# Performance work log

Measured on AMD Instinct MI355X. Metric: run time of the kernel, lower is better.

## Reference

```python
import math
import jax, jax.numpy as jnp
import numpy as np

NUM_CODE = 4096
CODE_DIM = 256
IN_DIM = 1024

def chi_dist_mean_std(c):
    mean = math.sqrt(2.0) * math.exp(math.lgamma((c + 1) / 2) - math.lgamma(c / 2))
    std = math.sqrt(c - mean ** 2)
    return mean, std

MU, SIGMA = chi_dist_mean_std(CODE_DIM)


def setup_inputs() -> dict:
    key = jax.random.key(0)
    k1, k2, k3 = jax.random.split(key, 3)
    encode = jax.random.normal(k1, (8, 64, 64, CODE_DIM), dtype=jnp.float32)
    codebook_w = jax.random.normal(k2, (NUM_CODE, IN_DIM), dtype=jnp.float32)  # N(0,1) init
    proj_w = jax.random.normal(k3, (CODE_DIM, IN_DIM), dtype=jnp.float32) * (1.0 / math.sqrt(IN_DIM))
    proj_b = jnp.zeros((CODE_DIM,), dtype=jnp.float32)
    return {"encode": encode, "codebook_w": codebook_w, "proj_w": proj_w, "proj_b": proj_b}


def _cdist(z, e):
    # pairwise euclidean distance: [T, K]
    z2 = jnp.sum(z * z, axis=-1, keepdims=True)          # [T,1]
    e2 = jnp.sum(e * e, axis=-1)[None, :]                # [1,K]
    d2 = z2 + e2 - 2.0 * jnp.einsum('tc,kc->tk', z, e)
    return jnp.sqrt(jnp.maximum(d2, 0.0))


def reference(encode, codebook_w, proj_w, proj_b):
    b, h, w, c = encode.shape
    e = codebook_w @ proj_w.T + proj_b                   # [K, code_dim]
    z = encode.reshape(-1, c)                            # [T, code_dim]
    s = -_cdist(z, e)                                    # [T, K] (computed under no_grad in torch)
    simi = (s.reshape(b, h, w, -1) - MU) / SIGMA
    zsoft = jax.nn.softmax(simi, axis=-1)                # eval path (std=0)
    zidx = jnp.argmax(zsoft, axis=-1)                    # [b,h,w]
    quant = e[zidx]                                      # [b,h,w,code_dim]
    return (zidx, quant)
```

## Files before the change

kernel.cpp:

```cpp
#include <hip/hip_runtime.h>
#include <hip/hip_bf16.h>


#define K_CODES 4096
#define CDIM    256
#define IDIM    1024
#define NTOK    32768

typedef __attribute__((ext_vector_type(8))) short short8;
typedef __attribute__((ext_vector_type(4))) float f32x4;

__device__ __forceinline__ unsigned short f32_to_bf16_rne(float f) {
  union { float f; unsigned int u; } x; x.f = f;
  unsigned int r = x.u + 0x7FFFu + ((x.u >> 16) & 1u);
  return (unsigned short)(r >> 16);
}
__device__ __forceinline__ float bf16_to_f32(unsigned short h) {
  union { unsigned int u; float f; } x; x.u = ((unsigned int)h) << 16;
  return x.f;
}

extern "C" __global__ __launch_bounds__(512)
void proj_gemm(const float* __restrict__ cb, const float* __restrict__ pw,
               const float* __restrict__ pb, float* __restrict__ e,
               unsigned short* __restrict__ Ect, float* __restrict__ e2p) {
  __shared__ float As[32][68];
  __shared__ float Bs[32][68];
  const int tid = threadIdx.x;
  const int tx = tid & 15, ty = tid >> 4;
  const int m0 = blockIdx.y << 6;
  const int n0 = blockIdx.x << 6;
  const int r  = tid >> 3;
  const int c4 = (tid & 7) << 2;
  float acc[2][4] = {};
  for (int k0 = 0; k0 < IDIM; k0 += 32) {
    float4 a0 = *(const float4*)&cb[(size_t)(m0 + r) * IDIM + k0 + c4];
    float4 b0 = *(const float4*)&pw[(size_t)(n0 + r) * IDIM + k0 + c4];
    __syncthreads();
    As[c4+0][r]=a0.x; As[c4+1][r]=a0.y; As[c4+2][r]=a0.z; As[c4+3][r]=a0.w;
    Bs[c4+0][r]=b0.x; Bs[c4+1][r]=b0.y; Bs[c4+2][r]=b0.z; Bs[c4+3][r]=b0.w;
    __syncthreads();
    #pragma unroll
    for (int kk = 0; kk < 32; ++kk) {
      const float2 av = *(const float2*)&As[kk][ty*2];
      const float4 bv = *(const float4*)&Bs[kk][tx*4];
      const float a2[2] = {av.x, av.y};
      const float b4[4] = {bv.x, bv.y, bv.z, bv.w};
      #pragma unroll
      for (int i = 0; i < 2; ++i)
        #pragma unroll
        for (int j = 0; j < 4; ++j)
          acc[i][j] += a2[i] * b4[j];
    }
  }
  const int col0 = n0 + tx*4;
  const int kb   = col0 >> 5;
  const int g    = (col0 >> 3) & 3;
  const int half = (col0 >> 2) & 1;
  float p2[2];
  #pragma unroll
  for (int i = 0; i < 2; ++i) {
    const int row = m0 + ty*2 + i;
    float vv[4];
    unsigned short h4[4], l4[4];
    #pragma unroll
    for (int j = 0; j < 4; ++j) {
      vv[j] = acc[i][j] + pb[col0 + j];
      h4[j] = f32_to_bf16_rne(vv[j]);
      l4[j] = f32_to_bf16_rne(vv[j] - bf16_to_f32(h4[j]));
    }
    *(float4*)&e[(size_t)row * CDIM + col0] = *(float4*)vv;
    const int ct = row >> 4, cl = row & 15;
    const size_t fi = ((size_t)(kb      * 256 + ct) * 64 + g*16 + cl) * 8 + half*4;
    const size_t fo = ((size_t)((kb+8)  * 256 + ct) * 64 + g*16 + cl) * 8 + half*4;
    *(ushort4*)&Ect[fi] = *(ushort4*)h4;
    *(ushort4*)&Ect[fo] = *(ushort4*)l4;
    p2[i] = vv[0]*vv[0] + vv[1]*vv[1] + vv[2]*vv[2] + vv[3]*vv[3];
  }
  #pragma unroll
  for (int m = 1; m < 16; m <<= 1) {
    p2[0] += __shfl_xor(p2[0], m, 64);
    p2[1] += __shfl_xor(p2[1], m, 64);
  }
  if (tx == 0) {
    e2p[(size_t)blockIdx.x * K_CODES + m0 + ty*2    ] = p2[0];
    e2p[(size_t)blockIdx.x * K_CODES + m0 + ty*2 + 1] = p2[1];
  }
}

extern "C" __global__ __launch_bounds__(512, 2)
void score_mfma(const float* __restrict__ z, const unsigned short* __restrict__ Ect,
                const float* __restrict__ e2p, const float* __restrict__ eg,
                float* __restrict__ zidx_f, float* __restrict__ quant) {
  extern __shared__ __align__(16) char smem[];
  char* Zb = smem;

  const int tid = threadIdx.x;
  const int l   = tid & 63;
  const int w   = tid >> 6;
  const int tg  = w >> 2;
  const int cg  = w & 3;
  const int t0  = blockIdx.x << 7;

  #pragma unroll
  for (int rr = 0; rr < 2; ++rr) {
    const int r  = rr*64 + (tid >> 3);
    const int cq = tid & 7;
    const int i8 = r >> 4;
    const int rl = (r & 15) << 4;
    #pragma unroll
    for (int it = 0; it < 4; ++it) {
      const int col = cq*32 + it*8;
      const float4 v0 = *(const float4*)&z[(size_t)(t0 + r) * CDIM + col];
      const float4 v1 = *(const float4*)&z[(size_t)(t0 + r) * CDIM + col + 4];
      float vv[8] = {v0.x,v0.y,v0.z,v0.w,v1.x,v1.y,v1.z,v1.w};
      unsigned int hp[4], lp[4];
      #pragma unroll
      for (int c = 0; c < 4; ++c) {
        unsigned short h0 = f32_to_bf16_rne(vv[2*c]);
        unsigned short h1 = f32_to_bf16_rne(vv[2*c+1]);
        unsigned short l0 = f32_to_bf16_rne(vv[2*c]   - bf16_to_f32(h0));
        unsigned short l1 = f32_to_bf16_rne(vv[2*c+1] - bf16_to_f32(h1));
        hp[c] = (unsigned int)h0 | ((unsigned int)h1 << 16);
        lp[c] = (unsigned int)l0 | ((unsigned int)l1 << 16);
      }
      const int lane_b = it*256 + rl;
      *(uint4*)(Zb + (size_t)(i8*16 + cq    ) * 1024 + lane_b) = *(uint4*)hp;
      *(uint4*)(Zb + (size_t)(i8*16 + cq + 8) * 1024 + lane_b) = *(uint4*)lp;
    }
  }
  __syncthreads();

  float bestv[4][4];
  int   besti[4][4];
  #pragma unroll
  for (int i = 0; i < 4; ++i)
    #pragma unroll
    for (int r = 0; r < 4; ++r) { bestv[i][r] = 3.4e38f; besti[i][r] = 0; }

  const int cl = l & 15;
  const int g  = l >> 4;

  const char* ebase = (const char*)Ect + (size_t)l * 16 + (size_t)cg * 4096;
  const char* Zl    = Zb + (size_t)l * 16 + (size_t)tg * 65536;

  short8 aHc[4], aLc[4], bHc[4], bLc[4];
  #pragma unroll
  for (int i = 0; i < 4; ++i) {
    aHc[i] = *(const short8*)(Zl + (size_t)(i*16 + 0) * 1024);
    aLc[i] = *(const short8*)(Zl + (size_t)(i*16 + 8) * 1024);
  }
  #pragma unroll
  for (int jj = 0; jj < 4; ++jj) {
    bHc[jj] = *(const short8*)(ebase + (size_t)0 * 262144 + jj * 1024);
    bLc[jj] = *(const short8*)(ebase + (size_t)8 * 262144 + jj * 1024);
  }

  for (int cc = 0; cc < 16; ++cc) {
    const char* ecc  = ebase + (size_t)cc * 16384;
    const char* eccn = ebase + (size_t)((cc + 1) & 15) * 16384;

    f32x4 acc[4][4];
    #pragma unroll
    for (int i = 0; i < 4; ++i)
      #pragma unroll
      for (int jj = 0; jj < 4; ++jj) acc[i][jj] = (f32x4){0.f,0.f,0.f,0.f};

    float e2v[4];
    #pragma unroll
    for (int jj = 0; jj < 4; ++jj) {
      const int code = cc*256 + cg*64 + jj*16 + cl;
      e2v[jj] = e2p[code] + e2p[K_CODES + code]
              + e2p[2*K_CODES + code] + e2p[3*K_CODES + code];
    }

    #pragma unroll
    for (int kw = 0; kw < 8; ++kw) {
      short8 aHn[4], aLn[4], bHn[4], bLn[4];
      {
        const char* bsrc = (kw < 7) ? ecc : eccn;
        const int kwn = (kw + 1) & 7;
        #pragma unroll
        for (int jj = 0; jj < 4; ++jj) {
          bHn[jj] = *(const short8*)(bsrc + (size_t)(kwn    ) * 262144 + jj * 1024);
          bLn[jj] = *(const short8*)(bsrc + (size_t)(kwn + 8) * 262144 + jj * 1024);
        }
        #pragma unroll
        for (int i = 0; i < 4; ++i) {
          aHn[i] = *(const short8*)(Zl + (size_t)(i*16 + kwn    ) * 1024);
          aLn[i] = *(const short8*)(Zl + (size_t)(i*16 + kwn + 8) * 1024);
        }
      }
      __builtin_amdgcn_s_setprio(1);
      #pragma unroll
      for (int i = 0; i < 4; ++i)
        #pragma unroll
        for (int jj = 0; jj < 4; ++jj)
          acc[i][jj] = __builtin_amdgcn_mfma_f32_16x16x32_bf16(aHc[i], bHc[jj], acc[i][jj], 0, 0, 0);
      #pragma unroll
      for (int i = 0; i < 4; ++i)
        #pragma unroll
        for (int jj = 0; jj < 4; ++jj)
          acc[i][jj] = __builtin_amdgcn_mfma_f32_16x16x32_bf16(aHc[i], bLc[jj], acc[i][jj], 0, 0, 0);
      #pragma unroll
      for (int i = 0; i < 4; ++i)
        #pragma unroll
        for (int jj = 0; jj < 4; ++jj)
          acc[i][jj] = __builtin_amdgcn_mfma_f32_16x16x32_bf16(aLc[i], bHc[jj], acc[i][jj], 0, 0, 0);
      __builtin_amdgcn_s_setprio(0);
      #pragma unroll
      for (int i = 0; i < 4; ++i) { aHc[i] = aHn[i]; aLc[i] = aLn[i]; }
      #pragma unroll
      for (int jj = 0; jj < 4; ++jj) { bHc[jj] = bHn[jj]; bLc[jj] = bLn[jj]; }
    }
    #pragma unroll
    for (int jj = 0; jj < 4; ++jj) {
      const int code = cc*256 + cg*64 + jj*16 + cl;
      #pragma unroll
      for (int i = 0; i < 4; ++i)
        #pragma unroll
        for (int r = 0; r < 4; ++r) {
          const float sc = e2v[jj] - 2.0f * acc[i][jj][r];
          if (sc < bestv[i][r]) { bestv[i][r] = sc; besti[i][r] = code; }
        }
    }
  }

  struct RP { float v; int i; };
  RP*  red    = (RP*)(smem + 131072);
  int* sh_idx = (int*)(smem + 131072 + 4096);
  #pragma unroll
  for (int i = 0; i < 4; ++i)
    #pragma unroll
    for (int r = 0; r < 4; ++r) {
      float v = bestv[i][r]; int bi = besti[i][r];
      #pragma unroll
      for (int m = 1; m < 16; m <<= 1) {
        const float ov = __shfl_xor(v, m, 64);
        const int   oi = __shfl_xor(bi, m, 64);
        if (ov < v || (ov == v && oi < bi)) { v = ov; bi = oi; }
      }
      if (cl == 0) {
        const int tl = tg*64 + i*16 + g*4 + r;
        red[tl*4 + cg].v = v; red[tl*4 + cg].i = bi;
      }
    }
  __syncthreads();
  if (tid < 128) {
    float v = red[tid*4].v; int bi = red[tid*4].i;
    #pragma unroll
    for (int x = 1; x < 4; ++x) {
      const float ov = red[tid*4 + x].v; const int oi = red[tid*4 + x].i;
      if (ov < v || (ov == v && oi < bi)) { v = ov; bi = oi; }
    }
    zidx_f[t0 + tid] = (float)bi;
    sh_idx[tid] = bi;
  }
  __syncthreads();

  #pragma unroll
  for (int rr = 0; rr < 2; ++rr) {
    const int r   = rr*64 + (tid >> 3);
    const int cq  = (tid & 7) << 5;
    const int idx = sh_idx[r];
    #pragma unroll
    for (int it = 0; it < 4; ++it) {
      const float4 v0 = *(const float4*)&eg[(size_t)idx * CDIM + cq + it*8];
      const float4 v1 = *(const float4*)&eg[(size_t)idx * CDIM + cq + it*8 + 4];
      *(float4*)&quant[(size_t)(t0 + r) * CDIM + cq + it*8]     = v0;
      *(float4*)&quant[(size_t)(t0 + r) * CDIM + cq + it*8 + 4] = v1;
    }
  }
}

extern "C" void kernel_launch(void* const* d_in, const int* in_sizes, int n_in,
                              void* d_out, int out_size, void* d_ws, size_t ws_size,
                              hipStream_t stream) {
  const float* encode = (const float*)d_in[0];
  const float* cb     = (const float*)d_in[1];
  const float* pw     = (const float*)d_in[2];
  const float* pb     = (const float*)d_in[3];

  float* e   = (float*)d_ws;
  float* e2p = e + (size_t)K_CODES * CDIM;
  unsigned short* Ect = (unsigned short*)(e2p + 4*K_CODES);

  float* out     = (float*)d_out;
  float* zidx_f  = out;
  float* quant_f = out + NTOK;

  (void)hipFuncSetAttribute((const void*)score_mfma,
                            hipFuncAttributeMaxDynamicSharedMemorySize, 135680);

  proj_gemm<<<dim3(CDIM/64, K_CODES/64), 512, 0, stream>>>(cb, pw, pb, e, Ect, e2p);
  score_mfma<<<NTOK/128, 512, 135680, stream>>>(encode, Ect, e2p, e, zidx_f, quant_f);
}
```

Measured before the change: 222.5 us.

## Split-K proj_gemm across two thread groups with 4x4 register tiles

The projection GEMM now splits the 1024-long reduction between two 256-thread halves of the block. Each thread computes a 4x4 output tile instead of 2x4, which raises arithmetic per shared-memory load. The two partial sums are combined through shared memory before the same epilogue (bias, bf16 hi/lo split, squared-norm partials). This aims to cut the loop trip count and improve register reuse, at the cost of more registers, a second shared buffer, and an extra reduction step with barriers.

Result: faster. 212.1 us (-4.7%).

```diff
diff --git a/kernel.cpp b/kernel.cpp
--- a/kernel.cpp
+++ b/kernel.cpp
@@ -24,67 +24,87 @@
 void proj_gemm(const float* __restrict__ cb, const float* __restrict__ pw,
                const float* __restrict__ pb, float* __restrict__ e,
                unsigned short* __restrict__ Ect, float* __restrict__ e2p) {
-  __shared__ float As[32][68];
-  __shared__ float Bs[32][68];
+  __shared__ float As[2][32][68];
+  __shared__ float Bs[2][32][68];
   const int tid = threadIdx.x;
-  const int tx = tid & 15, ty = tid >> 4;
-  const int m0 = blockIdx.y << 6;
-  const int n0 = blockIdx.x << 6;
-  const int r  = tid >> 3;
-  const int c4 = (tid & 7) << 2;
-  float acc[2][4] = {};
-  for (int k0 = 0; k0 < IDIM; k0 += 32) {
-    float4 a0 = *(const float4*)&cb[(size_t)(m0 + r) * IDIM + k0 + c4];
-    float4 b0 = *(const float4*)&pw[(size_t)(n0 + r) * IDIM + k0 + c4];
+  const int kg  = tid >> 8;
+  const int t   = tid & 255;
+  const int tx  = t & 15, ty = t >> 4;
+  const int m0  = blockIdx.y << 6;
+  const int n0  = blockIdx.x << 6;
+  const int r   = t >> 2;
+  const int c8  = (t & 3) << 3;
+  float acc[4][4] = {};
+  for (int k0s = 0; k0s < 16; ++k0s) {
+    const int k0 = kg*512 + k0s*32;
+    float4 a0 = *(const float4*)&cb[(size_t)(m0 + r) * IDIM + k0 + c8];
+    float4 a1 = *(const float4*)&cb[(size_t)(m0 + r) * IDIM + k0 + c8 + 4];
+    float4 b0 = *(const float4*)&pw[(size_t)(n0 + r) * IDIM + k0 + c8];
+    float4 b1 = *(const float4*)&pw[(size_t)(n0 + r) * IDIM + k0 + c8 + 4];
     __syncthreads();
-    As[c4+0][r]=a0.x; As[c4+1][r]=a0.y; As[c4+2][r]=a0.z; As[c4+3][r]=a0.w;
-    Bs[c4+0][r]=b0.x; Bs[c4+1][r]=b0.y; Bs[c4+2][r]=b0.z; Bs[c4+3][r]=b0.w;
+    As[kg][c8+0][r]=a0.x; As[kg][c8+1][r]=a0.y; As[kg][c8+2][r]=a0.z; As[kg][c8+3][r]=a0.w;
+    As[kg][c8+4][r]=a1.x; As[kg][c8+5][r]=a1.y; As[kg][c8+6][r]=a1.z; As[kg][c8+7][r]=a1.w;
+    Bs[kg][c8+0][r]=b0.x; Bs[kg][c8+1][r]=b0.y; Bs[kg][c8+2][r]=b0.z; Bs[kg][c8+3][r]=b0.w;
+    Bs[kg][c8+4][r]=b1.x; Bs[kg][c8+5][r]=b1.y; Bs[kg][c8+6][r]=b1.z; Bs[kg][c8+7][r]=b1.w;
     __syncthreads();
     #pragma unroll
     for (int kk = 0; kk < 32; ++kk) {
-      const float2 av = *(const float2*)&As[kk][ty*2];
-      const float4 bv = *(const float4*)&Bs[kk][tx*4];
-      const float a2[2] = {av.x, av.y};
+      const float4 av = *(const float4*)&As[kg][kk][ty*4];
+      const float4 bv = *(const float4*)&Bs[kg][kk][tx*4];
+      const float a4[4] = {av.x, av.y, av.z, av.w};
       const float b4[4] = {bv.x, bv.y, bv.z, bv.w};
       #pragma unroll
-      for (int i = 0; i < 2; ++i)
+      for (int i = 0; i < 4; ++i)
         #pragma unroll
         for (int j = 0; j < 4; ++j)
-          acc[i][j] += a2[i] * b4[j];
-    }
-  }
-  const int col0 = n0 + tx*4;
-  const int kb   = col0 >> 5;
-  const int g    = (col0 >> 3) & 3;
-  const int half = (col0 >> 2) & 1;
-  float p2[2];
-  #pragma unroll
-  for (int i = 0; i < 2; ++i) {
-    const int row = m0 + ty*2 + i;
-    float vv[4];
-    unsigned short h4[4], l4[4];
-    #pragma unroll
-    for (int j = 0; j < 4; ++j) {
-      vv[j] = acc[i][j] + pb[col0 + j];
-      h4[j] = f32_to_bf16_rne(vv[j]);
-      l4[j] = f32_to_bf16_rne(vv[j] - bf16_to_f32(h4[j]));
-    }
-    *(float4*)&e[(size_t)row * CDIM + col0] = *(float4*)vv;
-    const int ct = row >> 4, cl = row & 15;
-    const size_t fi = ((size_t)(kb      * 256 + ct) * 64 + g*16 + cl) * 8 + half*4;
-    const size_t fo = ((size_t)((kb+8)  * 256 + ct) * 64 + g*16 + cl) * 8 + half*4;
-    *(ushort4*)&Ect[fi] = *(ushort4*)h4;
-    *(ushort4*)&Ect[fo] = *(ushort4*)l4;
-    p2[i] = vv[0]*vv[0] + vv[1]*vv[1] + vv[2]*vv[2] + vv[3]*vv[3];
-  }
-  #pragma unroll
-  for (int m = 1; m < 16; m <<= 1) {
-    p2[0] += __shfl_xor(p2[0], m, 64);
-    p2[1] += __shfl_xor(p2[1], m, 64);
-  }
-  if (tx == 0) {
-    e2p[(size_t)blockIdx.x * K_CODES + m0 + ty*2    ] = p2[0];
-    e2p[(size_t)blockIdx.x * K_CODES + m0 + ty*2 + 1] = p2[1];
+          acc[i][j] += a4[i] * b4[j];
+    }
+  }
+  float* Cb = (float*)As;
+  __syncthreads();
+  if (kg == 1) {
+    #pragma unroll
+    for (int i = 0; i < 4; ++i)
+      *(float4*)&Cb[(ty*4 + i) * 64 + tx*4] = *(float4*)&acc[i][0];
+  }
+  __syncthreads();
+  if (kg == 0) {
+    const int col0 = n0 + tx*4;
+    const int kb   = col0 >> 5;
+    const int g    = (col0 >> 3) & 3;
+    const int half = (col0 >> 2) & 1;
+    float p2[4];
+    #pragma unroll
+    for (int i = 0; i < 4; ++i) {
+      const float4 o = *(const float4*)&Cb[(ty*4 + i) * 64 + tx*4];
+      const int row = m0 + ty*4 + i;
+      float vv[4];
+      unsigned short h4[4], l4[4];
+      const float o4[4] = {o.x, o.y, o.z, o.w};
+      #pragma unroll
+      for (int j = 0; j < 4; ++j) {
+        vv[j] = acc[i][j] + o4[j] + pb[col0 + j];
+        h4[j] = f32_to_bf16_rne(vv[j]);
+        l4[j] = f32_to_bf16_rne(vv[j] - bf16_to_f32(h4[j]));
+      }
+      *(float4*)&e[(size_t)row * CDIM + col0] = *(float4*)vv;
+      const int ct = row >> 4, cl = row & 15;
+      const size_t fi = ((size_t)(kb      * 256 + ct) * 64 + g*16 + cl) * 8 + half*4;
+      const size_t fo = ((size_t)((kb+8)  * 256 + ct) * 64 + g*16 + cl) * 8 + half*4;
+      *(ushort4*)&Ect[fi] = *(ushort4*)h4;
+      *(ushort4*)&Ect[fo] = *(ushort4*)l4;
+      p2[i] = vv[0]*vv[0] + vv[1]*vv[1] + vv[2]*vv[2] + vv[3]*vv[3];
+    }
+    #pragma unroll
+    for (int m = 1; m < 16; m <<= 1) {
+      #pragma unroll
+      for (int i = 0; i < 4; ++i) p2[i] += __shfl_xor(p2[i], m, 64);
+    }
+    if (tx == 0) {
+      #pragma unroll
+      for (int i = 0; i < 4; ++i)
+        e2p[(size_t)blockIdx.x * K_CODES + m0 + ty*4 + i] = p2[i];
+    }
   }
 }
 
```
